# Kernel optimization log

Measured on AMD Instinct MI355X. Metric: run time of the kernel, lower is better.

The kernel has to match this reference:

```python
import jax, jax.numpy as jnp
import numpy as np

B, L, D, H, K = 8, 2048, 1024, 16, 31
D_CONV = D // H  # 64
EPS = 1e-6


def setup_inputs() -> dict:
    key = jax.random.key(0)
    ks = jax.random.split(key, 5)
    return {
        "x": jax.random.normal(ks[0], (B, L, D), dtype=jnp.float32),
        "W_pe": (jax.random.normal(ks[1], (D_CONV, 2 * K), dtype=jnp.float32) * 0.1),
        "b_pe": jnp.zeros((2 * K,), dtype=jnp.float32),
        "stt_energy": jnp.ones((1, H, 1, K), dtype=jnp.float32)
                      + 0.02 * jax.random.normal(ks[2], (1, H, 1, K), dtype=jnp.float32),
        "W_fc": jax.random.normal(ks[3], (D, D), dtype=jnp.float32) / jnp.sqrt(jnp.float32(D)),
        "gamma": jnp.ones((D,), dtype=jnp.float32),
        "beta": jnp.zeros((D,), dtype=jnp.float32),
    }


def reference(x, W_pe, b_pe, stt_energy, W_fc, gamma, beta):
    b, l, d_model = x.shape
    d = d_model // H
    residual = x

    # mask_table matmul == causal running mean: avg[t] = mean(x[0..t])
    avg = jnp.cumsum(x, axis=1) / jnp.arange(1, l + 1, dtype=x.dtype)[None, :, None]

    # (B, L, H, d) -> (B*H, L, d)
    ci = avg.reshape(b, l, H, d).transpose(0, 2, 1, 3).reshape(b * H, l, d)

    pc = ci @ W_pe + b_pe                      # (BH, L, 2K)
    dyn, gate = pc[..., :K], pc[..., K:]
    stt = jnp.broadcast_to(stt_energy, (b, H, 1, K)).reshape(b * H, 1, K)
    energy = stt + jax.nn.sigmoid(gate) * dyn  # (BH, L, K)

    # as_strided banded softmax: energy[t,k] attends position t+k-(K-1);
    # -10000 fillers underflow to 0 in fp32, and out-of-range (negative position)
    # weights are dropped WITHOUT renormalization, as in the original slicing.
    w = jax.nn.softmax(energy, axis=-1)        # (BH, L, K)
    t_idx = jnp.arange(l)[:, None]
    k_idx = jnp.arange(K)[None, :]
    w = jnp.where(t_idx + k_idx - (K - 1) >= 0, w, jnp.zeros((), x.dtype))

    # banded bmm: out[t] = sum_k w[t,k] * ci[t+k-(K-1)]
    padded = jnp.pad(ci, ((0, 0), (K - 1, 0), (0, 0)))  # (BH, L+K-1, d)
    out = jnp.zeros((b * H, l, d), dtype=x.dtype)
    for kk in range(K):  # small fixed kernel-size loop
        out = out + w[:, :, kk:kk + 1] * padded[:, kk:kk + l, :]

    conv_loc = out.reshape(b, H, l, d).transpose(0, 2, 1, 3).reshape(b, l, d_model)

    v = conv_loc @ W_fc.T + residual
    mu = jnp.mean(v, axis=-1, keepdims=True)
    var = jnp.var(v, axis=-1, keepdims=True)
    v = (v - mu) / jnp.sqrt(var + EPS) * gamma + beta
    return v
```

## Files before the change

kernel.cpp:

```cpp
#include <hip/hip_runtime.h>
#include <math.h>

#define BB 8
#define LL 2048
#define DD 1024
#define HH 16
#define DH 64
#define KK 31
#define NSEG 32
#define SEGLEN 64

#define TLEN 64
#define TROW 2080
#define TSTR2 112
#define WBSTR2 104
#define WPESTR2 72
#define PCSS 64

typedef __attribute__((ext_vector_type(8))) short bf16x8;
typedef __attribute__((ext_vector_type(4))) float f32x4;
typedef __attribute__((ext_vector_type(8))) unsigned short u16x8;

__device__ __forceinline__ unsigned short f2bf(float f) {
    unsigned u = __float_as_uint(f);
    unsigned r = (u + 0x7fffu + ((u >> 16) & 1u)) >> 16;
    return (unsigned short)r;
}
__device__ __forceinline__ float bf2f(unsigned short s) {
    return __uint_as_float(((unsigned)s) << 16);
}

__device__ __forceinline__ void gload_lds16(const void* g, void* l) {
    __builtin_amdgcn_global_load_lds(
        (const __attribute__((address_space(1))) void*)g,
        (__attribute__((address_space(3))) void*)l, 16, 0, 0);
}

__global__ __launch_bounds__(256)
void seg_sum_kernel(const float* __restrict__ x, float* __restrict__ segsum) {
    int g = blockIdx.x * 256 + threadIdx.x;
    int d = g & (DD - 1);
    int s = (g >> 10) & (NSEG - 1);
    int b = g >> 15;
    const float* p = x + (size_t)(b * LL + s * SEGLEN) * DD + d;
    float acc = 0.f;
    #pragma unroll 8
    for (int i = 0; i < SEGLEN; ++i) acc += p[(size_t)i * DD];
    segsum[g] = acc;
}

__global__ __launch_bounds__(256)
void avg_kernel(const float* __restrict__ x, const float* __restrict__ segsum,
                unsigned short* __restrict__ avgT) {
    int g = blockIdx.x * 256 + threadIdx.x;
    int d = g & (DD - 1);
    int s = (g >> 10) & (NSEG - 1);
    int b = g >> 15;
    float run = 0.f;
    const float* ss = segsum + ((size_t)b << 15) + d;
    for (int s2 = 0; s2 < s; ++s2) run += ss[s2 << 10];
    const float* p = x + (size_t)(b * LL + s * SEGLEN) * DD + d;
    unsigned short* rowt = avgT +
        ((size_t)(b * HH + (d >> 6)) * DH + (d & 63)) * TROW;
    unsigned short* qt = rowt + 32 + s * SEGLEN;
    if (s == 0) {
        u16x8 z = {};
        #pragma unroll
        for (int j = 0; j < 4; ++j) *(u16x8*)&rowt[j * 8] = z;
    }
    int t0 = s * SEGLEN;
    #pragma unroll
    for (int j = 0; j < 8; ++j) {
        u16x8 v;
        #pragma unroll
        for (int e = 0; e < 8; ++e) {
            int i = j * 8 + e;
            run += p[(size_t)i * DD];
            v[e] = f2bf(run / (float)(t0 + i + 1));
        }
        *(u16x8*)&qt[j * 8] = v;
    }
}

__global__ __launch_bounds__(256, 4)
void conv_kernel(const unsigned short* __restrict__ avgT,
                 const unsigned short* __restrict__ wpeT,
                 const float* __restrict__ b_pe, const float* __restrict__ stt,
                 unsigned short* __restrict__ conv) {
    __shared__ __align__(16) unsigned short pcs[64 * PCSS];
    __shared__ __align__(16) unsigned short winT[64 * TSTR2];
    __shared__ __align__(16) unsigned short wub[64 * WBSTR2];

    int tid = threadIdx.x;
    int tile = blockIdx.x & 31;
    int bh = blockIdx.x >> 5;
    int b = bh >> 4, h = bh & 15;
    int t0 = tile * TLEN;
    int wv = tid >> 6, ln = tid & 63;
    int g = ln >> 4, li = ln & 15;

    {
        const unsigned short* gT = avgT + (size_t)(b * HH + h) * DH * TROW;
        #pragma unroll
        for (int q = 0; q < 3; ++q) {
            int i = tid + q * 256;
            int d = i / 14, c = i - d * 14;
            gload_lds16(gT + (size_t)d * TROW + t0 + c * 8, winT + (i & ~63) * 8);
        }
        if (tid < 128) {
            int i = 768 + tid;
            int d = i / 14, c = i - d * 14;
            gload_lds16(gT + (size_t)d * TROW + t0 + c * 8, winT + (i & ~63) * 8);
        }
        #pragma unroll
        for (int q = 0; q < 2; ++q) {
            int i = tid + q * 256;
            gload_lds16(wpeT + i * 8, wub + (i & ~63) * 8);
        }
        if (tid < 64) {
            int i = 512 + tid;
            gload_lds16(wpeT + i * 8, wub + (i & ~63) * 8);
        }
    }
    __syncthreads();

    f32x4 pacc[4];
    {
        int q32 = 32 + wv * 16 + li;
        bf16x8 a0, a1;
        #pragma unroll
        for (int e = 0; e < 8; ++e) {
            a0[e] = (short)winT[(g * 8 + e) * TSTR2 + q32];
            a1[e] = (short)winT[(32 + g * 8 + e) * TSTR2 + q32];
        }
        #pragma unroll
        for (int n = 0; n < 4; ++n) {
            int c = n * 16 + li;
            bf16x8 b0 = *(const bf16x8*)&wub[c * WPESTR2 + g * 8];
            bf16x8 b1 = *(const bf16x8*)&wub[c * WPESTR2 + 32 + g * 8];
            f32x4 z = {0.f, 0.f, 0.f, 0.f};
            z = __builtin_amdgcn_mfma_f32_16x16x32_bf16(a0, b0, z, 0, 0, 0);
            z = __builtin_amdgcn_mfma_f32_16x16x32_bf16(a1, b1, z, 0, 0, 0);
            pacc[n] = z;
        }
    }
    __syncthreads();

    {
        #pragma unroll
        for (int n = 0; n < 4; ++n) {
            int c = n * 16 + li;
            float bp = (c < 2 * KK) ? b_pe[c] : 0.f;
            #pragma unroll
            for (int r = 0; r < 4; ++r)
                pcs[(wv * 16 + g * 4 + r) * PCSS + c] = f2bf(pacc[n][r] + bp);
        }
        for (int i = tid; i < 64 * WBSTR2 / 8; i += 256) {
            u16x8 z = {};
            *(u16x8*)&wub[i * 8] = z;
        }
    }
    __syncthreads();

    {
        int half = ln >> 5, k = ln & 31;
        int kc = (k < KK) ? k : 0;
        float sttk = stt[h * KK + kc];
        for (int it = 0; it < 8; ++it) {
            int tok = wv * 16 + it * 2 + half;
            float dyn  = bf2f(pcs[tok * PCSS + kc]);
            float gate = bf2f(pcs[tok * PCSS + KK + kc]);
            float e = 0.f;
            if (k < KK) e = __expf(sttk + dyn / (1.f + __expf(-gate)));
            float sum = e;
            #pragma unroll
            for (int off = 16; off; off >>= 1) sum += __shfl_xor(sum, off, 64);
            float wvl = e / sum;
            if (k < KK && t0 + tok + k >= KK - 1)
                wub[tok * WBSTR2 + tok + k + 2] = f2bf(wvl);
        }
    }
    __syncthreads();

    {
        int row = wv * 16 + li;
        bf16x8 wa0 = *(const bf16x8*)&wub[row * WBSTR2 + g * 8];
        bf16x8 wa1 = *(const bf16x8*)&wub[row * WBSTR2 + 32 + g * 8];
        bf16x8 wa2 = *(const bf16x8*)&wub[row * WBSTR2 + 64 + g * 8];
        f32x4 cacc[4];
        #pragma unroll
        for (int n = 0; n < 4; ++n) {
            int c = n * 16 + li;
            bf16x8 b0 = *(const bf16x8*)&winT[c * TSTR2 + g * 8];
            bf16x8 b1 = *(const bf16x8*)&winT[c * TSTR2 + 32 + g * 8];
            bf16x8 b2 = *(const bf16x8*)&winT[c * TSTR2 + 64 + g * 8];
            f32x4 z = {0.f, 0.f, 0.f, 0.f};
            z = __builtin_amdgcn_mfma_f32_16x16x32_bf16(wa0, b0, z, 0, 0, 0);
            z = __builtin_amdgcn_mfma_f32_16x16x32_bf16(wa1, b1, z, 0, 0, 0);
            z = __builtin_amdgcn_mfma_f32_16x16x32_bf16(wa2, b2, z, 0, 0, 0);
            cacc[n] = z;
        }
        #pragma unroll
        for (int n = 0; n < 4; ++n)
            #pragma unroll
            for (int r = 0; r < 4; ++r)
                pcs[(wv * 16 + g * 4 + r) * PCSS + n * 16 + li] =
                    f2bf(cacc[n][r]);
    }
    __syncthreads();

    {
        int tok = tid >> 2, j0 = (tid & 3) * 16;
        u16x8 v0 = *(const u16x8*)&pcs[tok * PCSS + j0];
        u16x8 v1 = *(const u16x8*)&pcs[tok * PCSS + j0 + 8];
        unsigned short* o = conv + (size_t)(b * LL + t0 + tok) * DD + h * DH + j0;
        *(u16x8*)&o[0] = v0;
        *(u16x8*)&o[8] = v1;
    }
}

__global__ __launch_bounds__(256)
void cvt_kernel(const float* __restrict__ in, unsigned short* __restrict__ out,
                const float* __restrict__ W_pe, unsigned short* __restrict__ wpeT) {
    if (blockIdx.x == 1024) {
        for (int i = threadIdx.x; i < 64 * WPESTR2; i += 256) {
            int c = i / WPESTR2, d = i - c * WPESTR2;
            float v = (c < 2 * KK && d < 64) ? W_pe[d * (2 * KK) + c] : 0.f;
            wpeT[i] = f2bf(v);
        }
        return;
    }
    int i = (blockIdx.x * 256 + threadIdx.x) * 4;
    float4 v = *(const float4*)&in[i];
    ushort4 o;
    o.x = f2bf(v.x); o.y = f2bf(v.y); o.z = f2bf(v.z); o.w = f2bf(v.w);
    *(ushort4*)&out[i] = o;
}

#define WAITV0() do { asm volatile("s_waitcnt vmcnt(0)" ::: "memory"); \
                      __builtin_amdgcn_sched_barrier(0); } while (0)
#define LGK0()   do { asm volatile("s_waitcnt lgkmcnt(0)" ::: "memory"); \
                      __builtin_amdgcn_sched_barrier(0); } while (0)
#define BAR()    do { __builtin_amdgcn_sched_barrier(0); \
                      __builtin_amdgcn_s_barrier(); \
                      __builtin_amdgcn_sched_barrier(0); } while (0)

__global__ __launch_bounds__(512, 2)
void gemm_mfma_kernel(const unsigned short* __restrict__ A,
                      const unsigned short* __restrict__ Bt,
                      const float* __restrict__ X,
                      unsigned short* __restrict__ Vb)
{
    __shared__ __align__(16) unsigned short As0[256 * 64];
    __shared__ __align__(16) unsigned short Bs0[256 * 64];
    __shared__ __align__(16) unsigned short As1[256 * 64];
    __shared__ __align__(16) unsigned short Bs1[256 * 64];
    int tid = threadIdx.x;
    int wv = tid >> 6, ln = tid & 63;
    int bid = blockIdx.x;
    int nbid = (bid & 7) * 32 + (bid >> 3);
    int bm0 = (nbid >> 2) * 256;
    int bn0 = (nbid & 3) * 256;
    int wr = wv >> 2, wc = wv & 3;

    const unsigned short* ga[4];
    const unsigned short* gb[4];
    int ldo[4];
    #pragma unroll
    for (int i = 0; i < 4; ++i) {
        int dci = i * 512 + wv * 64 + ln;
        int row = dci >> 3, ch = dci & 7;
        int sc = ch ^ (row & 7);
        ga[i] = A  + (size_t)(bm0 + row) * 1024 + sc * 8;
        gb[i] = Bt + (size_t)(bn0 + row) * 1024 + sc * 8;
        ldo[i] = dci * 8;
    }

    f32x4 acc[8][4] = {};
    int la = wr * 128 + (ln & 15);
    int lb = wc * 64 + (ln & 15);
    int kg = ln >> 4;

#define READ_BFR(RB)                                                          \
    _Pragma("unroll")                                                         \
    for (int n = 0; n < 4; ++n)                                               \
      _Pragma("unroll")                                                       \
      for (int ks = 0; ks < 2; ++ks) {                                        \
        int row = lb + n * 16;                                                \
        bfr[n][ks] = *(const bf16x8*)&RB[row * 64 +                           \
                        (((kg + ks * 4) ^ (row & 7)) * 8)];                   \
      }

#define READ_AF(RA, MQ)                                                       \
    _Pragma("unroll")                                                         \
    for (int mm = 0; mm < 2; ++mm)                                            \
      _Pragma("unroll")                                                       \
      for (int ks = 0; ks < 2; ++ks) {                                        \
        int row = la + ((MQ) * 2 + mm) * 16;                                  \
        af[mm][ks] = *(const bf16x8*)&RA[row * 64 +                           \
                        (((kg + ks * 4) ^ (row & 7)) * 8)];                   \
      }

#define MFMAQ(MQ)                                                             \
    __builtin_amdgcn_s_setprio(1);                                            \
    _Pragma("unroll")                                                         \
    for (int mm = 0; mm < 2; ++mm)                                            \
      _Pragma("unroll")                                                       \
      for (int n = 0; n < 4; ++n)                                             \
        _Pragma("unroll")                                                     \
        for (int ks = 0; ks < 2; ++ks)                                        \
          acc[(MQ) * 2 + mm][n] = __builtin_amdgcn_mfma_f32_16x16x32_bf16(    \
              af[mm][ks], bfr[n][ks], acc[(MQ) * 2 + mm][n], 0, 0, 0);        \
    __builtin_amdgcn_s_setprio(0);

    #pragma unroll
    for (int i = 0; i < 4; ++i) {
        gload_lds16(ga[i], As0 + ldo[i]);
        gload_lds16(gb[i], Bs0 + ldo[i]);
    }
    WAITV0(); BAR();

    unsigned short* Ac = As0; unsigned short* Bc = Bs0;
    unsigned short* An = As1; unsigned short* Bn = Bs1;
    for (int t = 0; t < 16; ++t) {
        int ktn = (t + 1) * 64;
        bool last = (t == 15);
        bf16x8 bfr[4][2], af[2][2];
        READ_BFR(Bc); READ_AF(Ac, 0);
        if (!last) { gload_lds16(ga[0] + ktn, An + ldo[0]);
                     gload_lds16(ga[1] + ktn, An + ldo[1]);
                     gload_lds16(gb[0] + ktn, Bn + ldo[0]);
                     gload_lds16(gb[1] + ktn, Bn + ldo[1]); }
        BAR(); LGK0();
        MFMAQ(0);
        BAR();
        READ_AF(Ac, 1);
        if (!last) { gload_lds16(ga[2] + ktn, An + ldo[2]);
                     gload_lds16(ga[3] + ktn, An + ldo[3]);
                     gload_lds16(gb[2] + ktn, Bn + ldo[2]);
                     gload_lds16(gb[3] + ktn, Bn + ldo[3]); }
        BAR(); LGK0();
        MFMAQ(1);
        BAR();
        READ_AF(Ac, 2);
        BAR(); LGK0();
        MFMAQ(2);
        BAR();
        READ_AF(Ac, 3);
        if (!last) WAITV0();
        BAR(); LGK0();
        MFMAQ(3);
        BAR();
        unsigned short* tA = Ac; Ac = An; An = tA;
        unsigned short* tB = Bc; Bc = Bn; Bn = tB;
    }
#undef READ_BFR
#undef READ_AF
#undef MFMAQ

    int rb0 = bm0 + wr * 128 + (ln >> 4) * 4;
    int cb0 = bn0 + wc * 64 + (ln & 15);
    #pragma unroll
    for (int m = 0; m < 8; ++m) {
        #pragma unroll
        for (int r = 0; r < 4; ++r) {
            int row = rb0 + m * 16 + r;
            size_t off = (size_t)row * 1024 + cb0;
            #pragma unroll
            for (int n = 0; n < 4; ++n)
                Vb[off + n * 16] = f2bf(acc[m][n][r] + X[off + n * 16]);
        }
    }
}

__global__ __launch_bounds__(256)
void ln_kernel(const unsigned short* __restrict__ Vb,
               const float* __restrict__ gamma,
               const float* __restrict__ beta,
               float* __restrict__ out) {
    __shared__ float red[8];
    int row = blockIdx.x;
    int tid = threadIdx.x;
    ushort4 vu = *(const ushort4*)&Vb[(size_t)row * 1024 + tid * 4];
    float v0 = bf2f(vu.x), v1 = bf2f(vu.y), v2 = bf2f(vu.z), v3 = bf2f(vu.w);
    float s = v0 + v1 + v2 + v3;
    float s2 = v0 * v0 + v1 * v1 + v2 * v2 + v3 * v3;
    #pragma unroll
    for (int off = 32; off; off >>= 1) {
        s  += __shfl_xor(s, off, 64);
        s2 += __shfl_xor(s2, off, 64);
    }
    if ((tid & 63) == 0) { red[(tid >> 6) * 2] = s; red[(tid >> 6) * 2 + 1] = s2; }
    __syncthreads();
    s  = red[0] + red[2] + red[4] + red[6];
    s2 = red[1] + red[3] + red[5] + red[7];
    float mu = s * (1.f / 1024.f);
    float var = s2 * (1.f / 1024.f) - mu * mu;
    float rs = rsqrtf(var + 1e-6f);
    float4 g  = *(const float4*)&gamma[tid * 4];
    float4 be = *(const float4*)&beta[tid * 4];
    float4 o = make_float4((v0 - mu) * rs * g.x + be.x,
                           (v1 - mu) * rs * g.y + be.y,
                           (v2 - mu) * rs * g.z + be.z,
                           (v3 - mu) * rs * g.w + be.w);
    *(float4*)&out[(size_t)row * 1024 + tid * 4] = o;
}

extern "C" void kernel_launch(void* const* d_in, const int* in_sizes, int n_in,
                              void* d_out, int out_size, void* d_ws, size_t ws_size,
                              hipStream_t stream) {
    const float* x     = (const float*)d_in[0];
    const float* W_pe  = (const float*)d_in[1];
    const float* b_pe  = (const float*)d_in[2];
    const float* stt   = (const float*)d_in[3];
    const float* W_fc  = (const float*)d_in[4];
    const float* gamma = (const float*)d_in[5];
    const float* beta  = (const float*)d_in[6];
    float* out = (float*)d_out;

    char* ws = (char*)d_ws;
    unsigned short* Vb    = (unsigned short*)ws;
    unsigned short* avgT  = (unsigned short*)(ws + (size_t)32 * 1024 * 1024);
    unsigned short* convb = (unsigned short*)(ws + (size_t)68 * 1024 * 1024);
    unsigned short* wfcb  = (unsigned short*)(ws + (size_t)100 * 1024 * 1024);
    unsigned short* wpeT  = (unsigned short*)(ws + (size_t)102 * 1024 * 1024);
    float*          segs  = (float*)(ws + (size_t)103 * 1024 * 1024);

    seg_sum_kernel<<<1024, 256, 0, stream>>>(x, segs);
    avg_kernel<<<1024, 256, 0, stream>>>(x, segs, avgT);
    cvt_kernel<<<1025, 256, 0, stream>>>(W_fc, wfcb, W_pe, wpeT);
    conv_kernel<<<4096, 256, 0, stream>>>(avgT, wpeT, b_pe, stt, convb);
    gemm_mfma_kernel<<<256, 512, 0, stream>>>(convb, wfcb, x, Vb);
    ln_kernel<<<16384, 256, 0, stream>>>(Vb, gamma, beta, out);
}
```

Measured before the change: 147.5 us.

## Stagger A/B tile prefetch across quarters with partial vmcnt waits in GEMM loop

Reorders the global-to-LDS prefetch in the MFMA GEMM main loop so B tiles are issued early and A row-groups are issued later, just as the matching row quarters of the current A buffer are consumed. Full vmcnt(0) drains are replaced with partial waits (vmcnt(2)/vmcnt(4)) so some loads stay in flight across barriers. The goal is to spread memory traffic over the iteration and cut stall time at the end-of-step wait. It relies on the A load order lining up with which LDS rows each quarter reads. If the counts are wrong this is a race that can produce wrong results.

Result: no change. 145.4 us (-1.4%).

```diff
diff --git a/kernel.cpp b/kernel.cpp
--- a/kernel.cpp
+++ b/kernel.cpp
@@ -238,6 +238,10 @@
 }
 
 #define WAITV0() do { asm volatile("s_waitcnt vmcnt(0)" ::: "memory"); \
+                      __builtin_amdgcn_sched_barrier(0); } while (0)
+#define WAITV2() do { asm volatile("s_waitcnt vmcnt(2)" ::: "memory"); \
+                      __builtin_amdgcn_sched_barrier(0); } while (0)
+#define WAITV4() do { asm volatile("s_waitcnt vmcnt(4)" ::: "memory"); \
                       __builtin_amdgcn_sched_barrier(0); } while (0)
 #define LGK0()   do { asm volatile("s_waitcnt lgkmcnt(0)" ::: "memory"); \
                       __builtin_amdgcn_sched_barrier(0); } while (0)
@@ -313,12 +317,15 @@
               af[mm][ks], bfr[n][ks], acc[(MQ) * 2 + mm][n], 0, 0, 0);        \
     __builtin_amdgcn_s_setprio(0);
 
-    #pragma unroll
-    for (int i = 0; i < 4; ++i) {
-        gload_lds16(ga[i], As0 + ldo[i]);
-        gload_lds16(gb[i], Bs0 + ldo[i]);
-    }
-    WAITV0(); BAR();
+    gload_lds16(gb[0], Bs0 + ldo[0]);
+    gload_lds16(gb[1], Bs0 + ldo[1]);
+    gload_lds16(gb[2], Bs0 + ldo[2]);
+    gload_lds16(gb[3], Bs0 + ldo[3]);
+    gload_lds16(ga[0], As0 + ldo[0]);
+    gload_lds16(ga[2], As0 + ldo[2]);
+    gload_lds16(ga[1], As0 + ldo[1]);
+    gload_lds16(ga[3], As0 + ldo[3]);
+    WAITV2(); BAR();
 
     unsigned short* Ac = As0; unsigned short* Bc = Bs0;
     unsigned short* An = As1; unsigned short* Bn = Bs1;
@@ -327,29 +334,30 @@
         bool last = (t == 15);
         bf16x8 bfr[4][2], af[2][2];
         READ_BFR(Bc); READ_AF(Ac, 0);
-        if (!last) { gload_lds16(ga[0] + ktn, An + ldo[0]);
-                     gload_lds16(ga[1] + ktn, An + ldo[1]);
-                     gload_lds16(gb[0] + ktn, Bn + ldo[0]);
+        if (!last) { gload_lds16(gb[0] + ktn, Bn + ldo[0]);
                      gload_lds16(gb[1] + ktn, Bn + ldo[1]); }
         BAR(); LGK0();
         MFMAQ(0);
         BAR();
         READ_AF(Ac, 1);
-        if (!last) { gload_lds16(ga[2] + ktn, An + ldo[2]);
-                     gload_lds16(ga[3] + ktn, An + ldo[3]);
-                     gload_lds16(gb[2] + ktn, Bn + ldo[2]);
+        if (!last) { gload_lds16(gb[2] + ktn, Bn + ldo[2]);
                      gload_lds16(gb[3] + ktn, Bn + ldo[3]); }
         BAR(); LGK0();
         MFMAQ(1);
+        if (last) { WAITV0(); } else { WAITV4(); }
         BAR();
         READ_AF(Ac, 2);
+        if (!last) { gload_lds16(ga[0] + ktn, An + ldo[0]);
+                     gload_lds16(ga[2] + ktn, An + ldo[2]); }
         BAR(); LGK0();
         MFMAQ(2);
         BAR();
         READ_AF(Ac, 3);
-        if (!last) WAITV0();
+        if (!last) { gload_lds16(ga[1] + ktn, An + ldo[1]);
+                     gload_lds16(ga[3] + ktn, An + ldo[3]); }
         BAR(); LGK0();
         MFMAQ(3);
+        if (!last) WAITV2();
         BAR();
         unsigned short* tA = Ac; Ac = An; An = tA;
         unsigned short* tB = Bc; Bc = Bn; Bn = tB;
```

## Use 4-wave GEMM blocks with 128x128 per-wave tiles and simpler double-buffer pipeline

Applied to the files above, without the earlier changes.

The GEMM block drops from 8 waves to 4, so each wave now computes a 128x128 output tile (8x8 MFMA accumulators) instead of 128x64. The fine-grained quarter-step schedule with many barriers is replaced by one full-tile prefetch per iteration, a partial vmcnt wait and a single MFMA pass over the current buffer. The aim is more operand reuse per LDS read and fewer barriers, at the cost of 256 accumulator registers per lane and less latency hiding from fewer waves.

New measurement: 156.0 us. 1.06x slower.

```diff
diff --git a/kernel.cpp b/kernel.cpp
--- a/kernel.cpp
+++ b/kernel.cpp
@@ -237,15 +237,15 @@
     *(ushort4*)&out[i] = o;
 }
 
-#define WAITV0() do { asm volatile("s_waitcnt vmcnt(0)" ::: "memory"); \
-                      __builtin_amdgcn_sched_barrier(0); } while (0)
-#define LGK0()   do { asm volatile("s_waitcnt lgkmcnt(0)" ::: "memory"); \
-                      __builtin_amdgcn_sched_barrier(0); } while (0)
-#define BAR()    do { __builtin_amdgcn_sched_barrier(0); \
-                      __builtin_amdgcn_s_barrier(); \
-                      __builtin_amdgcn_sched_barrier(0); } while (0)
-
-__global__ __launch_bounds__(512, 2)
+#define WAITV0()  do { asm volatile("s_waitcnt vmcnt(0)" ::: "memory"); \
+                       __builtin_amdgcn_sched_barrier(0); } while (0)
+#define WAITV16() do { asm volatile("s_waitcnt vmcnt(16)" ::: "memory"); \
+                       __builtin_amdgcn_sched_barrier(0); } while (0)
+#define BAR()     do { __builtin_amdgcn_sched_barrier(0); \
+                       __builtin_amdgcn_s_barrier(); \
+                       __builtin_amdgcn_sched_barrier(0); } while (0)
+
+__global__ __launch_bounds__(256, 1)
 void gemm_mfma_kernel(const unsigned short* __restrict__ A,
                       const unsigned short* __restrict__ Bt,
                       const float* __restrict__ X,
@@ -261,105 +261,65 @@
     int nbid = (bid & 7) * 32 + (bid >> 3);
     int bm0 = (nbid >> 2) * 256;
     int bn0 = (nbid & 3) * 256;
-    int wr = wv >> 2, wc = wv & 3;
-
-    const unsigned short* ga[4];
-    const unsigned short* gb[4];
-    int ldo[4];
-    #pragma unroll
-    for (int i = 0; i < 4; ++i) {
-        int dci = i * 512 + wv * 64 + ln;
-        int row = dci >> 3, ch = dci & 7;
-        int sc = ch ^ (row & 7);
-        ga[i] = A  + (size_t)(bm0 + row) * 1024 + sc * 8;
-        gb[i] = Bt + (size_t)(bn0 + row) * 1024 + sc * 8;
-        ldo[i] = dci * 8;
-    }
-
-    f32x4 acc[8][4] = {};
+    int wr = wv >> 1, wc = wv & 1;
+
+    int srow = tid >> 3;
+    int sc = (tid & 7) ^ (srow & 7);
+    const unsigned short* ga0 = A  + (size_t)(bm0 + srow) * 1024 + sc * 8;
+    const unsigned short* gb0 = Bt + (size_t)(bn0 + srow) * 1024 + sc * 8;
+    int ldo0 = tid * 8;
+
+    f32x4 acc[8][8] = {};
     int la = wr * 128 + (ln & 15);
-    int lb = wc * 64 + (ln & 15);
+    int lb = wc * 128 + (ln & 15);
     int kg = ln >> 4;
-
-#define READ_BFR(RB)                                                          \
-    _Pragma("unroll")                                                         \
-    for (int n = 0; n < 4; ++n)                                               \
-      _Pragma("unroll")                                                       \
+    int rxor = (ln & 7) * 8;
+
+#define STAGE(SA, SB, kt)                                           \
+    { _Pragma("unroll")                                             \
+      for (int i = 0; i < 8; ++i) {                                 \
+          gload_lds16(ga0 + i * 32768 + (kt), SA + ldo0 + i * 2048);\
+          gload_lds16(gb0 + i * 32768 + (kt), SB + ldo0 + i * 2048);\
+      } }
+
+#define MFMA_TILE(RA, RB)                                                     \
+    { _Pragma("unroll")                                                       \
       for (int ks = 0; ks < 2; ++ks) {                                        \
-        int row = lb + n * 16;                                                \
-        bfr[n][ks] = *(const bf16x8*)&RB[row * 64 +                           \
-                        (((kg + ks * 4) ^ (row & 7)) * 8)];                   \
-      }
-
-#define READ_AF(RA, MQ)                                                       \
-    _Pragma("unroll")                                                         \
-    for (int mm = 0; mm < 2; ++mm)                                            \
-      _Pragma("unroll")                                                       \
-      for (int ks = 0; ks < 2; ++ks) {                                        \
-        int row = la + ((MQ) * 2 + mm) * 16;                                  \
-        af[mm][ks] = *(const bf16x8*)&RA[row * 64 +                           \
-                        (((kg + ks * 4) ^ (row & 7)) * 8)];                   \
-      }
-
-#define MFMAQ(MQ)                                                             \
-    __builtin_amdgcn_s_setprio(1);                                            \
-    _Pragma("unroll")                                                         \
-    for (int mm = 0; mm < 2; ++mm)                                            \
-      _Pragma("unroll")                                                       \
-      for (int n = 0; n < 4; ++n)                                             \
-        _Pragma("unroll")                                                     \
-        for (int ks = 0; ks < 2; ++ks)                                        \
-          acc[(MQ) * 2 + mm][n] = __builtin_amdgcn_mfma_f32_16x16x32_bf16(    \
-              af[mm][ks], bfr[n][ks], acc[(MQ) * 2 + mm][n], 0, 0, 0);        \
-    __builtin_amdgcn_s_setprio(0);
-
-    #pragma unroll
-    for (int i = 0; i < 4; ++i) {
-        gload_lds16(ga[i], As0 + ldo[i]);
-        gload_lds16(gb[i], Bs0 + ldo[i]);
-    }
-    WAITV0(); BAR();
-
+          int cko = (((kg + ks * 4) * 8) ^ rxor);                             \
+          bf16x8 bfr[8];                                                      \
+          _Pragma("unroll")                                                   \
+          for (int n = 0; n < 8; ++n)                                         \
+              bfr[n] = *(const bf16x8*)&RB[(lb + n * 16) * 64 + cko];         \
+          _Pragma("unroll")                                                   \
+          for (int m = 0; m < 8; ++m) {                                       \
+              bf16x8 af = *(const bf16x8*)&RA[(la + m * 16) * 64 + cko];      \
+              __builtin_amdgcn_s_setprio(1);                                  \
+              _Pragma("unroll")                                               \
+              for (int n = 0; n < 8; ++n)                                     \
+                  acc[m][n] = __builtin_amdgcn_mfma_f32_16x16x32_bf16(        \
+                      af, bfr[n], acc[m][n], 0, 0, 0);                        \
+              __builtin_amdgcn_s_setprio(0);                                  \
+          }                                                                   \
+      } }
+
+    STAGE(As0, Bs0, 0);
     unsigned short* Ac = As0; unsigned short* Bc = Bs0;
     unsigned short* An = As1; unsigned short* Bn = Bs1;
     for (int t = 0; t < 16; ++t) {
-        int ktn = (t + 1) * 64;
         bool last = (t == 15);
-        bf16x8 bfr[4][2], af[2][2];
-        READ_BFR(Bc); READ_AF(Ac, 0);
-        if (!last) { gload_lds16(ga[0] + ktn, An + ldo[0]);
-                     gload_lds16(ga[1] + ktn, An + ldo[1]);
-                     gload_lds16(gb[0] + ktn, Bn + ldo[0]);
-                     gload_lds16(gb[1] + ktn, Bn + ldo[1]); }
-        BAR(); LGK0();
-        MFMAQ(0);
+        if (!last) STAGE(An, Bn, (t + 1) * 64);
+        if (last) { WAITV0(); } else { WAITV16(); }
         BAR();
-        READ_AF(Ac, 1);
-        if (!last) { gload_lds16(ga[2] + ktn, An + ldo[2]);
-                     gload_lds16(ga[3] + ktn, An + ldo[3]);
-                     gload_lds16(gb[2] + ktn, Bn + ldo[2]);
-                     gload_lds16(gb[3] + ktn, Bn + ldo[3]); }
-        BAR(); LGK0();
-        MFMAQ(1);
-        BAR();
-        READ_AF(Ac, 2);
-        BAR(); LGK0();
-        MFMAQ(2);
-        BAR();
-        READ_AF(Ac, 3);
-        if (!last) WAITV0();
-        BAR(); LGK0();
-        MFMAQ(3);
+        MFMA_TILE(Ac, Bc);
         BAR();
         unsigned short* tA = Ac; Ac = An; An = tA;
         unsigned short* tB = Bc; Bc = Bn; Bn = tB;
     }
-#undef READ_BFR
-#undef READ_AF
-#undef MFMAQ
+#undef STAGE
+#undef MFMA_TILE
 
     int rb0 = bm0 + wr * 128 + (ln >> 4) * 4;
-    int cb0 = bn0 + wc * 64 + (ln & 15);
+    int cb0 = bn0 + wc * 128 + (ln & 15);
     #pragma unroll
     for (int m = 0; m < 8; ++m) {
         #pragma unroll
@@ -367,7 +327,7 @@
             int row = rb0 + m * 16 + r;
             size_t off = (size_t)row * 1024 + cb0;
             #pragma unroll
-            for (int n = 0; n < 4; ++n)
+            for (int n = 0; n < 8; ++n)
                 Vb[off + n * 16] = f2bf(acc[m][n][r] + X[off + n * 16]);
         }
     }
@@ -430,6 +390,6 @@
     avg_kernel<<<1024, 256, 0, stream>>>(x, segs, avgT);
     cvt_kernel<<<1025, 256, 0, stream>>>(W_fc, wfcb, W_pe, wpeT);
     conv_kernel<<<4096, 256, 0, stream>>>(avgT, wpeT, b_pe, stt, convb);
-    gemm_mfma_kernel<<<256, 512, 0, stream>>>(convb, wfcb, x, Vb);
+    gemm_mfma_kernel<<<256, 256, 0, stream>>>(convb, wfcb, x, Vb);
     ln_kernel<<<16384, 256, 0, stream>>>(Vb, gamma, beta, out);
 }
```
